# Kernel optimization log

Measured on AMD Instinct MI355X. Metric: run time of the kernel, lower is better.

Reference implementation:

```python
import jax, jax.numpy as jnp
import numpy as np

N_NODES = 100000
N_EDGES = 1600000
D_IN, D_HID, D_LAT = 128, 128, 64


def setup_inputs() -> dict:
    key = jax.random.key(0)
    ks = jax.random.split(key, 8)
    x = jax.random.normal(ks[0], (N_NODES, D_IN), dtype=jnp.float32)
    edge_index = jax.random.randint(ks[1], (2, N_EDGES), 0, N_NODES, dtype=jnp.int64)
    s1 = 1.0 / np.sqrt(D_IN)
    s2 = 1.0 / np.sqrt(D_HID)
    return {
        "x": x,
        "edge_index": edge_index,
        "W1_l": jax.random.normal(ks[2], (D_IN, D_HID), dtype=jnp.float32) * s1,
        "W1_r": jax.random.normal(ks[3], (D_IN, D_HID), dtype=jnp.float32) * s1,
        "b1": jnp.zeros((D_HID,), dtype=jnp.float32),
        "W2_l": jax.random.normal(ks[4], (D_HID, D_LAT), dtype=jnp.float32) * s2,
        "W2_r": jax.random.normal(ks[5], (D_HID, D_LAT), dtype=jnp.float32) * s2,
        "b2": jnp.zeros((D_LAT,), dtype=jnp.float32),
    }


def _sage_conv_mean(x, src, dst, W_l, W_r, b):
    """PyG SAGEConv with mean aggregation: lin_l(mean_j x_j) + lin_r(x_i)."""
    n = x.shape[0]
    # scatter-mean of source features into destination nodes
    agg = jax.ops.segment_sum(x[src], dst, num_segments=n)           # [N, d]
    deg = jax.ops.segment_sum(jnp.ones_like(dst, dtype=x.dtype), dst, num_segments=n)
    mean = agg / jnp.maximum(deg, 1.0)[:, None]
    return mean @ W_l + b + x @ W_r


def reference(x, edge_index, W1_l, W1_r, b1, W2_l, W2_r, b2):
    src, dst = edge_index[0], edge_index[1]
    h = jax.nn.relu(_sage_conv_mean(x, src, dst, W1_l, W1_r, b1))
    # Dropout(p=0.2) is identity in eval mode
    z = jax.nn.relu(_sage_conv_mean(h, src, dst, W2_l, W2_r, b2))
    return z
```

## Files before the change

### kernel.cpp

```cpp
#include <hip/hip_runtime.h>

#define N_NODES 100000
#define N_EDGES 1600000
#define D_IN 128
#define D_HID 128
#define D_LAT 64

#define BSHIFT 8
#define NB 392
#define CAP 4608
#define EPB 4096
#define PART_BLOCKS ((N_EDGES + EPB - 1) / EPB)
#define CVT_BLOCKS (((long)N_NODES * 128 / 16 + 255) / 256)

typedef unsigned short ushort_t;
typedef unsigned int uint_t;
typedef unsigned char uchar_t;
using bf16x8 = __attribute__((ext_vector_type(8))) short;
using f32x4  = __attribute__((ext_vector_type(4))) float;
using f32x2  = __attribute__((ext_vector_type(2))) float;

__device__ inline ushort_t f2bf(float f) {
    uint_t u = __float_as_uint(f);
    return (ushort_t)((u + 0x7fffu + ((u >> 16) & 1u)) >> 16);
}
__device__ inline uint_t pack2bf(float a, float b) {
    return (uint_t)f2bf(a) | ((uint_t)f2bf(b) << 16);
}
__device__ inline float bf2f(ushort_t u) {
    return __uint_as_float(((uint_t)u) << 16);
}

#if __has_builtin(__builtin_amdgcn_cvt_pk_f32_fp8) && __has_builtin(__builtin_amdgcn_cvt_pk_fp8_f32)
#define HW_FP8 1
template<bool HI>
__device__ inline f32x2 fp8pk2f(uint_t v) {
    return __builtin_amdgcn_cvt_pk_f32_fp8(v, HI);
}
__device__ inline uint_t f2fp8pk4(float a, float b, float c, float d) {
    uint_t w = __builtin_amdgcn_cvt_pk_fp8_f32(a, b, 0, false);
    w = __builtin_amdgcn_cvt_pk_fp8_f32(c, d, w, true);
    return w;
}
__device__ inline uchar_t f2fp8_byte(float f) {
    return (uchar_t)(__builtin_amdgcn_cvt_pk_fp8_f32(f, f, 0, false) & 0xff);
}
#else
__device__ inline float fp8b2f(uint_t b) {
    uint_t em = b & 0x7f;
    if (em == 0) return 0.f;
    uint_t bits = ((em << 20) + (120u << 23)) | ((b & 0x80u) << 24);
    return __uint_as_float(bits);
}
template<bool HI>
__device__ inline f32x2 fp8pk2f(uint_t v) {
    uint_t w = HI ? (v >> 16) : v;
    f32x2 r; r.x = fp8b2f(w & 0xff); r.y = fp8b2f((w >> 8) & 0xff);
    return r;
}
__device__ inline uint_t f2fp8_1(float f) {
    uint_t u = __float_as_uint(f);
    uint_t s = (u >> 31) << 7;
    uint_t au = u & 0x7fffffff;
    if (au >= 0x43e00000u) return s | 0x7e;
    if (au < 0x3c000000u) return s;
    uint_t r = au + 0x0007ffffu + ((au >> 20) & 1u);
    return s | (((r >> 20) - (120u << 3)) & 0x7f);
}
__device__ inline uint_t f2fp8pk4(float a, float b, float c, float d) {
    return f2fp8_1(a) | (f2fp8_1(b) << 8) | (f2fp8_1(c) << 16) | (f2fp8_1(d) << 24);
}
__device__ inline uchar_t f2fp8_byte(float f) { return (uchar_t)f2fp8_1(f); }
#endif

__device__ inline void accf8x4(float* a, uint_t w, int base) {
    f32x2 p0 = fp8pk2f<false>(w);
    f32x2 p1 = fp8pk2f<true>(w);
    a[base + 0] += p0.x; a[base + 1] += p0.y;
    a[base + 2] += p1.x; a[base + 3] += p1.y;
}
__device__ inline void accf8x16(float* a, uint4 u) {
    accf8x4(a, u.x, 0); accf8x4(a, u.y, 4); accf8x4(a, u.z, 8); accf8x4(a, u.w, 12);
}

template<int RSHIFT, int NV, int DEPTH>
__device__ inline void gather_acc_fp8n(const uchar_t* __restrict__ base,
                                       const int* __restrict__ idxp,
                                       int n, float* acc) {
    int k = 0;
    int idx[DEPTH];
    if (n >= DEPTH) {
        #pragma unroll
        for (int j = 0; j < DEPTH; ++j) idx[j] = idxp[j];
    }
    while (k + DEPTH <= n) {
        uint4 u[DEPTH][NV];
        #pragma unroll
        for (int j = 0; j < DEPTH; ++j) {
            #pragma unroll
            for (int v = 0; v < NV; ++v)
                u[j][v] = *(const uint4*)(base + ((long)idx[j] << RSHIFT) + v * 16);
        }
        int kn = k + DEPTH;
        if (kn + DEPTH <= n) {
            #pragma unroll
            for (int j = 0; j < DEPTH; ++j) idx[j] = idxp[kn + j];
        }
        #pragma unroll
        for (int j = 0; j < DEPTH; ++j) {
            #pragma unroll
            for (int v = 0; v < NV; ++v)
                accf8x16(acc + v * 16, u[j][v]);
        }
        k = kn;
    }
    if (k < n) {
        int m = n - k;
        int idr[DEPTH];
        #pragma unroll
        for (int j = 0; j < DEPTH; ++j) {
            int kk = k + j; if (kk > n - 1) kk = n - 1;
            idr[j] = idxp[kk];
        }
        uint4 u[DEPTH][NV];
        #pragma unroll
        for (int j = 0; j < DEPTH; ++j) {
            #pragma unroll
            for (int v = 0; v < NV; ++v)
                u[j][v] = *(const uint4*)(base + ((long)idr[j] << RSHIFT) + v * 16);
        }
        #pragma unroll
        for (int j = 0; j < DEPTH; ++j) {
            if (j < m) {
                #pragma unroll
                for (int v = 0; v < NV; ++v)
                    accf8x16(acc + v * 16, u[j][v]);
            }
        }
    }
}

__device__ inline void pack_w256(const float* Wl, const float* Wr, ushort_t* pack,
                                 int N, int tid) {
    int lane = tid & 63;
    int t = tid >> 6;
    int kt = t & 7;
    int nt = t >> 3;
    int n = nt * 16 + (lane & 15);
    int kbase = kt * 32 + (lane >> 4) * 8;
    ushort_t v[8];
    #pragma unroll
    for (int j = 0; j < 8; ++j) {
        int k = kbase + j;
        float w = (k < 128) ? Wl[k * N + n] : Wr[(k - 128) * N + n];
        v[j] = f2bf(w);
    }
    *(uint4*)(pack + (long)tid * 8) = *(uint4*)v;
}
__device__ inline void pack_w128(const float* W, ushort_t* pack, int N, int tid) {
    int lane = tid & 63;
    int t = tid >> 6;
    int kt = t & 3;
    int nt = t >> 2;
    int n = nt * 16 + (lane & 15);
    int kbase = kt * 32 + (lane >> 4) * 8;
    ushort_t v[8];
    #pragma unroll
    for (int j = 0; j < 8; ++j) v[j] = f2bf(W[(kbase + j) * N + n]);
    *(uint4*)(pack + (long)tid * 8) = *(uint4*)v;
}

__global__ __launch_bounds__(256) void prep_kernel(
        const float* __restrict__ W1_l, const float* __restrict__ W1_r,
        ushort_t* __restrict__ pack1,
        const float* __restrict__ W2_l, ushort_t* __restrict__ pack2l,
        const float* __restrict__ W2_r, ushort_t* __restrict__ pack2r,
        int* __restrict__ gCur,
        const float* __restrict__ x, ushort_t* __restrict__ xb,
        uchar_t* __restrict__ x8) {
    int b = blockIdx.x;
    if (b < 16) {
        pack_w256(W1_l, W1_r, pack1, 128, b * 256 + threadIdx.x);
    } else if (b < 20) {
        pack_w128(W2_l, pack2l, 64, (b - 16) * 256 + threadIdx.x);
    } else if (b < 24) {
        pack_w128(W2_r, pack2r, 64, (b - 20) * 256 + threadIdx.x);
    } else if (b < 26) {
        int t = (b - 24) * 256 + threadIdx.x;
        if (t < NB) gCur[t] = t * CAP;
    } else {
        long i = ((long)(b - 26) * 256 + threadIdx.x) * 16;
        if (i >= (long)N_NODES * 128) return;
        float4 a = *(const float4*)(x + i);
        float4 bb = *(const float4*)(x + i + 4);
        float4 c = *(const float4*)(x + i + 8);
        float4 d = *(const float4*)(x + i + 12);
        uint4 ob0, ob1;
        ob0.x = pack2bf(a.x, a.y);  ob0.y = pack2bf(a.z, a.w);
        ob0.z = pack2bf(bb.x, bb.y); ob0.w = pack2bf(bb.z, bb.w);
        ob1.x = pack2bf(c.x, c.y);  ob1.y = pack2bf(c.z, c.w);
        ob1.z = pack2bf(d.x, d.y);  ob1.w = pack2bf(d.z, d.w);
        *(uint4*)(xb + i) = ob0;
        *(uint4*)(xb + i + 8) = ob1;
        uint4 o8;
        o8.x = f2fp8pk4(a.x, a.y, a.z, a.w);
        o8.y = f2fp8pk4(bb.x, bb.y, bb.z, bb.w);
        o8.z = f2fp8pk4(c.x, c.y, c.z, c.w);
        o8.w = f2fp8pk4(d.x, d.y, d.z, d.w);
        *(uint4*)(x8 + i) = o8;
    }
}

__global__ __launch_bounds__(256) void bucket_scatter_kernel(const int* __restrict__ src,
                                                             const int* __restrict__ dst,
                                                             int* __restrict__ gCur,
                                                             int* __restrict__ bedges) {
    __shared__ int h[NB];
    __shared__ int start[NB];
    for (int j = threadIdx.x; j < NB; j += 256) h[j] = 0;
    __syncthreads();
    long base = (long)blockIdx.x * EPB + threadIdx.x * 16;
    int dc[16], sc[16];
    int cnt = 0;
    if (base + 16 <= N_EDGES) {
        #pragma unroll
        for (int j = 0; j < 4; ++j) {
            int4 d4 = *(const int4*)(dst + base + j * 4);
            int4 s4 = *(const int4*)(src + base + j * 4);
            dc[j * 4 + 0] = d4.x; dc[j * 4 + 1] = d4.y; dc[j * 4 + 2] = d4.z; dc[j * 4 + 3] = d4.w;
            sc[j * 4 + 0] = s4.x; sc[j * 4 + 1] = s4.y; sc[j * 4 + 2] = s4.z; sc[j * 4 + 3] = s4.w;
        }
        cnt = 16;
    } else if (base < N_EDGES) {
        cnt = (int)(N_EDGES - base);
        for (int j = 0; j < cnt; ++j) { dc[j] = dst[base + j]; sc[j] = src[base + j]; }
    }
    for (int j = 0; j < cnt; ++j) atomicAdd(&h[dc[j] >> BSHIFT], 1);
    __syncthreads();
    for (int j = threadIdx.x; j < NB; j += 256)
        start[j] = h[j] ? atomicAdd(&gCur[j], h[j]) : 0;
    __syncthreads();
    for (int j = 0; j < cnt; ++j) {
        int b = dc[j] >> BSHIFT;
        int p = atomicAdd(&start[b], 1);
        if (p < (b + 1) * CAP)
            bedges[p] = ((dc[j] & 255) << 24) | sc[j];
    }
}

__global__ __launch_bounds__(256) void bucket_sort_kernel(const int* __restrict__ gCur,
                                                          const int* __restrict__ bedges,
                                                          int* __restrict__ csr,
                                                          int2* __restrict__ off2) {
    __shared__ int sdata[256];
    __shared__ int cur[256];
    int b = blockIdx.x, t = threadIdx.x;
    int r0 = b * CAP;
    int n = gCur[b] - r0;
    if (n > CAP) n = CAP;
    cur[t] = 0;
    __syncthreads();
    for (int k = t * 4; k < n; k += 1024) {
        int4 v4 = *(const int4*)(bedges + r0 + k);
        int m = n - k;
        atomicAdd(&cur[(unsigned)v4.x >> 24], 1);
        if (m > 1) atomicAdd(&cur[(unsigned)v4.y >> 24], 1);
        if (m > 2) atomicAdd(&cur[(unsigned)v4.z >> 24], 1);
        if (m > 3) atomicAdd(&cur[(unsigned)v4.w >> 24], 1);
    }
    __syncthreads();
    int c = cur[t];
    sdata[t] = c;
    __syncthreads();
    for (int d = 1; d < 256; d <<= 1) {
        int u = (t >= d) ? sdata[t - d] : 0;
        __syncthreads();
        sdata[t] += u;
        __syncthreads();
    }
    int ex = (t == 0) ? 0 : sdata[t - 1];
    off2[(b << BSHIFT) + t] = make_int2(r0 + ex, c);
    cur[t] = ex;
    __syncthreads();
    for (int k = t * 4; k < n; k += 1024) {
        int4 v4 = *(const int4*)(bedges + r0 + k);
        int m = n - k;
        {
            int p = atomicAdd(&cur[(unsigned)v4.x >> 24], 1);
            csr[r0 + p] = v4.x & 0xFFFFFF;
        }
        if (m > 1) {
            int p = atomicAdd(&cur[(unsigned)v4.y >> 24], 1);
            csr[r0 + p] = v4.y & 0xFFFFFF;
        }
        if (m > 2) {
            int p = atomicAdd(&cur[(unsigned)v4.z >> 24], 1);
            csr[r0 + p] = v4.z & 0xFFFFFF;
        }
        if (m > 3) {
            int p = atomicAdd(&cur[(unsigned)v4.w >> 24], 1);
            csr[r0 + p] = v4.w & 0xFFFFFF;
        }
    }
}

#define HSTRIDE 132
__global__ __launch_bounds__(256) void mfma_mlp_fused_kernel(
        const int2* __restrict__ off2, const int* __restrict__ csr_src,
        const uchar_t* __restrict__ x8,
        const ushort_t* __restrict__ Ax,
        const ushort_t* __restrict__ pack1, const float* __restrict__ bias,
        const ushort_t* __restrict__ pack2l,
        ushort_t* __restrict__ hb, uchar_t* __restrict__ g8) {
    __shared__ ushort_t mtile[64 * HSTRIDE];
    __shared__ ushort_t htile[4][16 * HSTRIDE];
    long m0b = (long)blockIdx.x * 64;
    {
        int lane4 = threadIdx.x & 3;
        int local = threadIdx.x >> 2;
        long i = m0b + local;
        if (i > N_NODES - 1) i = N_NODES - 1;
        int2 bd = off2[i];
        const uchar_t* gbase = x8 + lane4 * 32;
        float acc[32];
        #pragma unroll
        for (int j = 0; j < 32; ++j) acc[j] = 0.f;
        gather_acc_fp8n<7, 2, 4>(gbase, csr_src + bd.x, bd.y, acc);
        float inv = (bd.y > 0) ? 1.f / (float)bd.y : 0.f;
        uint_t o[8];
        #pragma unroll
        for (int j = 0; j < 8; ++j)
            o[j] = pack2bf(acc[j * 2] * inv, acc[j * 2 + 1] * inv);
        ushort_t* mp = mtile + local * HSTRIDE + lane4 * 32;
        *(uint4*)mp = *(uint4*)o;
        *(uint4*)(mp + 8) = *(uint4*)(o + 4);
        uint_t o2[8];
        #pragma unroll
        for (int j = 0; j < 8; ++j)
            o2[j] = pack2bf(acc[16 + j * 2] * inv, acc[16 + j * 2 + 1] * inv);
        *(uint4*)(mp + 16) = *(uint4*)o2;
        *(uint4*)(mp + 24) = *(uint4*)(o2 + 4);
    }
    __syncthreads();
    int lane = threadIdx.x & 63;
    int wave = threadIdx.x >> 6;
    long m0 = m0b + wave * 16;
    int r = lane & 15;
    int quad = lane >> 4;
    long arow = m0 + r;
    if (arow > N_NODES - 1) arow = N_NODES - 1;
    int rowl = wave * 16 + r;

    bf16x8 areg[8];
    #pragma unroll
    for (int kt = 0; kt < 8; ++kt) {
        int k = (kt & 3) * 32 + quad * 8;
        areg[kt] = (kt < 4)
            ? *(const bf16x8*)(&mtile[rowl * HSTRIDE + k])
            : *(const bf16x8*)(Ax + arow * 128 + k);
    }

    f32x4 acc[8];
    #pragma unroll
    for (int nt = 0; nt < 8; ++nt) acc[nt] = (f32x4){0.f, 0.f, 0.f, 0.f};
    #pragma unroll
    for (int nt = 0; nt < 8; ++nt) {
        #pragma unroll
        for (int kt = 0; kt < 8; ++kt) {
            bf16x8 bfrag = *(const bf16x8*)(pack1 + ((long)(nt * 8 + kt) * 64 + lane) * 8);
            acc[nt] = __builtin_amdgcn_mfma_f32_16x16x32_bf16(areg[kt], bfrag, acc[nt], 0, 0, 0);
        }
    }

    #pragma unroll
    for (int nt = 0; nt < 8; ++nt) {
        int col = nt * 16 + r;
        float bj = bias[col];
        #pragma unroll
        for (int q = 0; q < 4; ++q) {
            long orow = m0 + quad * 4 + q;
            float v = fmaxf(acc[nt][q] + bj, 0.f);
            ushort_t hv = f2bf(v);
            if (orow < N_NODES) hb[orow * 128 + col] = hv;
            htile[wave][(quad * 4 + q) * HSTRIDE + col] = hv;
        }
    }
    bf16x8 areg2[4];
    #pragma unroll
    for (int kt = 0; kt < 4; ++kt)
        areg2[kt] = *(const bf16x8*)(&htile[wave][r * HSTRIDE + kt * 32 + quad * 8]);
    f32x4 gacc[4];
    #pragma unroll
    for (int nt = 0; nt < 4; ++nt) gacc[nt] = (f32x4){0.f, 0.f, 0.f, 0.f};
    #pragma unroll
    for (int nt = 0; nt < 4; ++nt) {
        #pragma unroll
        for (int kt = 0; kt < 4; ++kt) {
            bf16x8 bfrag = *(const bf16x8*)(pack2l + ((long)(nt * 4 + kt) * 64 + lane) * 8);
            gacc[nt] = __builtin_amdgcn_mfma_f32_16x16x32_bf16(areg2[kt], bfrag, gacc[nt], 0, 0, 0);
        }
    }
    #pragma unroll
    for (int nt = 0; nt < 4; ++nt) {
        int col = nt * 16 + r;
        #pragma unroll
        for (int q = 0; q < 4; ++q) {
            long orow = m0 + quad * 4 + q;
            if (orow < N_NODES) g8[orow * 64 + col] = f2fp8_byte(gacc[nt][q]);
        }
    }
}

#define MSTRIDE 68
__global__ __launch_bounds__(256) void mfma_final_kernel(
        const int2* __restrict__ off2, const int* __restrict__ csr_src,
        const uchar_t* __restrict__ g8,
        const ushort_t* __restrict__ hb, const ushort_t* __restrict__ pack2r,
        const float* __restrict__ b2, float* __restrict__ out) {
    __shared__ ushort_t mtile[64 * MSTRIDE];
    long m0 = (long)blockIdx.x * 64;
    {
        int lane  = threadIdx.x & 3;
        int local = threadIdx.x >> 2;
        long i = m0 + local;
        if (i > N_NODES - 1) i = N_NODES - 1;
        int2 bd = off2[i];
        int beg = bd.x, n = bd.y;
        const uchar_t* base = g8 + lane * 16;
        float acc[16];
        #pragma unroll
        for (int j = 0; j < 16; ++j) acc[j] = 0.f;
        gather_acc_fp8n<6, 1, 8>(base, csr_src + beg, n, acc);
        float inv = (n > 0) ? 1.f / (float)n : 0.f;
        uint4 o0, o1;
        o0.x = pack2bf(acc[0] * inv,  acc[1] * inv);
        o0.y = pack2bf(acc[2] * inv,  acc[3] * inv);
        o0.z = pack2bf(acc[4] * inv,  acc[5] * inv);
        o0.w = pack2bf(acc[6] * inv,  acc[7] * inv);
        o1.x = pack2bf(acc[8] * inv,  acc[9] * inv);
        o1.y = pack2bf(acc[10] * inv, acc[11] * inv);
        o1.z = pack2bf(acc[12] * inv, acc[13] * inv);
        o1.w = pack2bf(acc[14] * inv, acc[15] * inv);
        ushort_t* mp = mtile + local * MSTRIDE + lane * 16;
        *(uint4*)mp = o0;
        *(uint4*)(mp + 8) = o1;
    }
    __syncthreads();
    int lane = threadIdx.x & 63;
    int wave = threadIdx.x >> 6;
    long mw = m0 + wave * 16;
    int r = lane & 15;
    int quad = lane >> 4;
    long arow = mw + r;
    if (arow > N_NODES - 1) arow = N_NODES - 1;

    bf16x8 areg[4];
    #pragma unroll
    for (int kt = 0; kt < 4; ++kt)
        areg[kt] = *(const bf16x8*)(hb + arow * 128 + kt * 32 + quad * 8);

    f32x4 acc[4];
    #pragma unroll
    for (int nt = 0; nt < 4; ++nt) {
        int col = nt * 16 + r;
        #pragma unroll
        for (int q = 0; q < 4; ++q) {
            int rowl = wave * 16 + quad * 4 + q;
            acc[nt][q] = bf2f(mtile[rowl * MSTRIDE + col]);
        }
    }
    #pragma unroll
    for (int nt = 0; nt < 4; ++nt) {
        #pragma unroll
        for (int kt = 0; kt < 4; ++kt) {
            bf16x8 bfrag = *(const bf16x8*)(pack2r + ((long)(nt * 4 + kt) * 64 + lane) * 8);
            acc[nt] = __builtin_amdgcn_mfma_f32_16x16x32_bf16(areg[kt], bfrag, acc[nt], 0, 0, 0);
        }
    }
    #pragma unroll
    for (int nt = 0; nt < 4; ++nt) {
        int col = nt * 16 + r;
        float bj = b2[col];
        #pragma unroll
        for (int q = 0; q < 4; ++q) {
            long orow = mw + quad * 4 + q;
            if (orow < N_NODES)
                out[orow * 64 + col] = fmaxf(acc[nt][q] + bj, 0.f);
        }
    }
}

extern "C" void kernel_launch(void* const* d_in, const int* in_sizes, int n_in,
                              void* d_out, int out_size, void* d_ws, size_t ws_size,
                              hipStream_t stream) {
    const float* x    = (const float*)d_in[0];
    const int*   ei   = (const int*)d_in[1];
    const float* W1_l = (const float*)d_in[2];
    const float* W1_r = (const float*)d_in[3];
    const float* b1   = (const float*)d_in[4];
    const float* W2_l = (const float*)d_in[5];
    const float* W2_r = (const float*)d_in[6];
    const float* b2   = (const float*)d_in[7];
    float* out = (float*)d_out;

    const int* src = ei;
    const int* dst = ei + N_EDGES;

    int*  gCur   = (int*)d_ws;
    int2* off2   = (int2*)(gCur + 512);
    int*  bedges = (int*)(off2 + 100608);
    int*  csr    = bedges + NB * CAP;
    ushort_t* xb = (ushort_t*)(csr + NB * CAP);
    ushort_t* hb = xb + (long)N_NODES * 128;
    uchar_t*  x8 = (uchar_t*)(hb + (long)N_NODES * 128);
    ushort_t* pack1  = (ushort_t*)(x8 + (long)N_NODES * 128);
    ushort_t* pack2l = pack1 + 256 * 128;
    ushort_t* pack2r = pack2l + 128 * 64;
    uchar_t*  g8     = (uchar_t*)(pack2r + 128 * 64);

    prep_kernel<<<26 + CVT_BLOCKS, 256, 0, stream>>>(
        W1_l, W1_r, pack1, W2_l, pack2l, W2_r, pack2r, gCur, x, xb, x8);

    bucket_scatter_kernel<<<PART_BLOCKS, 256, 0, stream>>>(src, dst, gCur, bedges);
    bucket_sort_kernel<<<NB, 256, 0, stream>>>(gCur, bedges, csr, off2);

    mfma_mlp_fused_kernel<<<(N_NODES + 63) / 64, 256, 0, stream>>>(
        off2, csr, x8, xb, pack1, b1, pack2l, hb, g8);

    mfma_final_kernel<<<(N_NODES + 63) / 64, 256, 0, stream>>>(
        off2, csr, g8, hb, pack2r, b2, out);
}
```

Baseline: 256.6 us.

## Shrink fused MLP tile to 32 rows with 8 lanes per node gather

The fused layer-1 kernel now handles 32 nodes per block instead of 64, using 8 threads per node with 16 features each for the neighbour gather. The four waves split into a 2x2 grid over rows and output columns, so each wave computes half the columns of both MLP stages, with a block barrier before the second stage reads the shared hidden tile. Bounds clamps are dropped because 100000 divides by 32. This doubles the block count and spreads the gather more finely, at the cost of an extra barrier and more redundant A-fragment loads per block.

After: 232.5 us. -9.4%, faster.

```diff
diff --git a/kernel.cpp b/kernel.cpp
--- a/kernel.cpp
+++ b/kernel.cpp
@@ -312,44 +312,42 @@
         const ushort_t* __restrict__ pack1, const float* __restrict__ bias,
         const ushort_t* __restrict__ pack2l,
         ushort_t* __restrict__ hb, uchar_t* __restrict__ g8) {
-    __shared__ ushort_t mtile[64 * HSTRIDE];
-    __shared__ ushort_t htile[4][16 * HSTRIDE];
-    long m0b = (long)blockIdx.x * 64;
+    __shared__ ushort_t mtile[32 * HSTRIDE];
+    __shared__ ushort_t htile[32 * HSTRIDE];
+    long m0b = (long)blockIdx.x * 32;
     {
-        int lane4 = threadIdx.x & 3;
-        int local = threadIdx.x >> 2;
+        int lane8 = threadIdx.x & 7;
+        int local = threadIdx.x >> 3;
         long i = m0b + local;
-        if (i > N_NODES - 1) i = N_NODES - 1;
         int2 bd = off2[i];
-        const uchar_t* gbase = x8 + lane4 * 32;
-        float acc[32];
-        #pragma unroll
-        for (int j = 0; j < 32; ++j) acc[j] = 0.f;
-        gather_acc_fp8n<7, 2, 4>(gbase, csr_src + bd.x, bd.y, acc);
+        const uchar_t* gbase = x8 + lane8 * 16;
+        float acc[16];
+        #pragma unroll
+        for (int j = 0; j < 16; ++j) acc[j] = 0.f;
+        gather_acc_fp8n<7, 1, 8>(gbase, csr_src + bd.x, bd.y, acc);
         float inv = (bd.y > 0) ? 1.f / (float)bd.y : 0.f;
-        uint_t o[8];
-        #pragma unroll
-        for (int j = 0; j < 8; ++j)
-            o[j] = pack2bf(acc[j * 2] * inv, acc[j * 2 + 1] * inv);
-        ushort_t* mp = mtile + local * HSTRIDE + lane4 * 32;
-        *(uint4*)mp = *(uint4*)o;
-        *(uint4*)(mp + 8) = *(uint4*)(o + 4);
-        uint_t o2[8];
-        #pragma unroll
-        for (int j = 0; j < 8; ++j)
-            o2[j] = pack2bf(acc[16 + j * 2] * inv, acc[16 + j * 2 + 1] * inv);
-        *(uint4*)(mp + 16) = *(uint4*)o2;
-        *(uint4*)(mp + 24) = *(uint4*)(o2 + 4);
+        uint4 o0, o1;
+        o0.x = pack2bf(acc[0] * inv,  acc[1] * inv);
+        o0.y = pack2bf(acc[2] * inv,  acc[3] * inv);
+        o0.z = pack2bf(acc[4] * inv,  acc[5] * inv);
+        o0.w = pack2bf(acc[6] * inv,  acc[7] * inv);
+        o1.x = pack2bf(acc[8] * inv,  acc[9] * inv);
+        o1.y = pack2bf(acc[10] * inv, acc[11] * inv);
+        o1.z = pack2bf(acc[12] * inv, acc[13] * inv);
+        o1.w = pack2bf(acc[14] * inv, acc[15] * inv);
+        ushort_t* mp = mtile + local * HSTRIDE + lane8 * 16;
+        *(uint4*)mp = o0;
+        *(uint4*)(mp + 8) = o1;
     }
     __syncthreads();
     int lane = threadIdx.x & 63;
     int wave = threadIdx.x >> 6;
-    long m0 = m0b + wave * 16;
+    int wr = wave & 1;
+    int wc = wave >> 1;
     int r = lane & 15;
     int quad = lane >> 4;
-    long arow = m0 + r;
-    if (arow > N_NODES - 1) arow = N_NODES - 1;
-    int rowl = wave * 16 + r;
+    int rowl = wr * 16 + r;
+    long arow = m0b + rowl;
 
     bf16x8 areg[8];
     #pragma unroll
@@ -360,53 +358,56 @@
             : *(const bf16x8*)(Ax + arow * 128 + k);
     }
 
-    f32x4 acc[8];
-    #pragma unroll
-    for (int nt = 0; nt < 8; ++nt) acc[nt] = (f32x4){0.f, 0.f, 0.f, 0.f};
-    #pragma unroll
-    for (int nt = 0; nt < 8; ++nt) {
+    f32x4 acc[4];
+    #pragma unroll
+    for (int nt = 0; nt < 4; ++nt) acc[nt] = (f32x4){0.f, 0.f, 0.f, 0.f};
+    #pragma unroll
+    for (int nt = 0; nt < 4; ++nt) {
+        int gnt = wc * 4 + nt;
         #pragma unroll
         for (int kt = 0; kt < 8; ++kt) {
-            bf16x8 bfrag = *(const bf16x8*)(pack1 + ((long)(nt * 8 + kt) * 64 + lane) * 8);
+            bf16x8 bfrag = *(const bf16x8*)(pack1 + ((long)(gnt * 8 + kt) * 64 + lane) * 8);
             acc[nt] = __builtin_amdgcn_mfma_f32_16x16x32_bf16(areg[kt], bfrag, acc[nt], 0, 0, 0);
         }
     }
 
     #pragma unroll
-    for (int nt = 0; nt < 8; ++nt) {
-        int col = nt * 16 + r;
+    for (int nt = 0; nt < 4; ++nt) {
+        int col = wc * 64 + nt * 16 + r;
         float bj = bias[col];
         #pragma unroll
         for (int q = 0; q < 4; ++q) {
-            long orow = m0 + quad * 4 + q;
+            long orow = m0b + wr * 16 + quad * 4 + q;
             float v = fmaxf(acc[nt][q] + bj, 0.f);
             ushort_t hv = f2bf(v);
-            if (orow < N_NODES) hb[orow * 128 + col] = hv;
-            htile[wave][(quad * 4 + q) * HSTRIDE + col] = hv;
-        }
-    }
+            hb[orow * 128 + col] = hv;
+            htile[(wr * 16 + quad * 4 + q) * HSTRIDE + col] = hv;
+        }
+    }
+    __syncthreads();
     bf16x8 areg2[4];
     #pragma unroll
     for (int kt = 0; kt < 4; ++kt)
-        areg2[kt] = *(const bf16x8*)(&htile[wave][r * HSTRIDE + kt * 32 + quad * 8]);
-    f32x4 gacc[4];
-    #pragma unroll
-    for (int nt = 0; nt < 4; ++nt) gacc[nt] = (f32x4){0.f, 0.f, 0.f, 0.f};
-    #pragma unroll
-    for (int nt = 0; nt < 4; ++nt) {
+        areg2[kt] = *(const bf16x8*)(&htile[rowl * HSTRIDE + kt * 32 + quad * 8]);
+    f32x4 gacc[2];
+    #pragma unroll
+    for (int nt = 0; nt < 2; ++nt) gacc[nt] = (f32x4){0.f, 0.f, 0.f, 0.f};
+    #pragma unroll
+    for (int nt = 0; nt < 2; ++nt) {
+        int gnt = wc * 2 + nt;
         #pragma unroll
         for (int kt = 0; kt < 4; ++kt) {
-            bf16x8 bfrag = *(const bf16x8*)(pack2l + ((long)(nt * 4 + kt) * 64 + lane) * 8);
+            bf16x8 bfrag = *(const bf16x8*)(pack2l + ((long)(gnt * 4 + kt) * 64 + lane) * 8);
             gacc[nt] = __builtin_amdgcn_mfma_f32_16x16x32_bf16(areg2[kt], bfrag, gacc[nt], 0, 0, 0);
         }
     }
     #pragma unroll
-    for (int nt = 0; nt < 4; ++nt) {
-        int col = nt * 16 + r;
+    for (int nt = 0; nt < 2; ++nt) {
+        int col = wc * 32 + nt * 16 + r;
         #pragma unroll
         for (int q = 0; q < 4; ++q) {
-            long orow = m0 + quad * 4 + q;
-            if (orow < N_NODES) g8[orow * 64 + col] = f2fp8_byte(gacc[nt][q]);
+            long orow = m0b + wr * 16 + quad * 4 + q;
+            g8[orow * 64 + col] = f2fp8_byte(gacc[nt][q]);
         }
     }
 }
@@ -524,7 +525,7 @@
     bucket_scatter_kernel<<<PART_BLOCKS, 256, 0, stream>>>(src, dst, gCur, bedges);
     bucket_sort_kernel<<<NB, 256, 0, stream>>>(gCur, bedges, csr, off2);
 
-    mfma_mlp_fused_kernel<<<(N_NODES + 63) / 64, 256, 0, stream>>>(
+    mfma_mlp_fused_kernel<<<N_NODES / 32, 256, 0, stream>>>(
         off2, csr, x8, xb, pack1, b1, pack2l, hb, g8);
 
     mfma_final_kernel<<<(N_NODES + 63) / 64, 256, 0, stream>>>(
```
